# Kernel optimization log

Measured on AMD Instinct MI355X. Metric: run time of the kernel, lower is better.

Reference implementation:

```python
import jax, jax.numpy as jnp
import numpy as np

B, T, C, H = 4, 4096, 1024, 16


def setup_inputs() -> dict:
    key = jax.random.key(0)
    k1, k2, k3 = jax.random.split(key, 3)
    x = jax.random.normal(k1, (B, T, C), dtype=jnp.float32)
    # nn.Linear(d_model, 3*d_model, bias=False): weight shape [3C, C]
    W_qkv = jax.random.normal(k2, (3 * C, C), dtype=jnp.float32) * 0.02
    # output Linear(d_model, d_model): weight [C, C], bias [C]
    W_out = jax.random.normal(k3, (C, C), dtype=jnp.float32) * 0.02
    b_out = jnp.zeros((C,), dtype=jnp.float32)
    return {"x": x, "W_qkv": W_qkv, "W_out": W_out, "b_out": b_out}


def reference(x, W_qkv, W_out, b_out):
    Bs, Ts, Cs = x.shape
    dh = Cs // H
    scale = dh ** (-0.5)
    # qkv projection: [B,T,3C]
    qkv = x @ W_qkv.T
    q, k, v = jnp.split(qkv, 3, axis=-1)

    def to_heads(t):  # [B,T,C] -> [B,H,T,dh]
        return t.reshape(Bs, Ts, H, dh).transpose(0, 2, 1, 3)

    q, k, v = to_heads(q), to_heads(k), to_heads(v)
    # rfft over the sequence dim -> [B,H,F,dh], F = T//2+1 (complex64)
    q_f = jnp.fft.rfft(q, axis=-2)
    k_f = jnp.fft.rfft(k, axis=-2)
    # spectral score: sum over head_dim of conj(q)*k, real part -> [B,H,F]
    attn = jnp.sum(jnp.conj(q_f) * k_f, axis=-1).real * scale
    attn = jax.nn.softmax(attn, axis=-1)  # softmax over frequency bins
    v_f = jnp.fft.rfft(v, axis=-2)
    out = jnp.fft.irfft(attn[..., None] * v_f, n=Ts, axis=-2)  # [B,H,T,dh]
    out = out.transpose(0, 2, 1, 3).reshape(Bs, Ts, Cs)
    # output projection (dropout is identity in eval)
    return out @ W_out.T + b_out
```

## Files before the change

### kernel.cpp

```cpp
#include <hip/hip_runtime.h>
#include <math.h>

#define Bsz   4
#define Tsz   4096
#define Csz   1024
#define Hn    16
#define DHn   64
#define NTOT  (Bsz * Tsz)
#define M3    (3 * Csz)
#define Fn    2049
#define BHn   (Bsz * Hn)
#define HALFN 8192

typedef __bf16 bf16x8 __attribute__((ext_vector_type(8)));
typedef __bf16 bf16x4 __attribute__((ext_vector_type(4)));
typedef float  f32x4  __attribute__((ext_vector_type(4)));

#define VMCNT(n) asm volatile("s_waitcnt vmcnt(" #n ")" ::: "memory")

__device__ __forceinline__ void gload_lds16(const void* g, void* l) {
  __builtin_amdgcn_global_load_lds(
      (const __attribute__((address_space(1))) void*)g,
      (__attribute__((address_space(3))) void*)l, 16, 0, 0);
}

__global__ __launch_bounds__(256)
void cvt_hilo_kernel(const float4* __restrict__ in, bf16x4* __restrict__ hi,
                     bf16x4* __restrict__ lo, int n4) {
  int i = blockIdx.x * blockDim.x + threadIdx.x;
  if (i >= n4) return;
  float4 v = in[i];
  bf16x4 h, l;
  h[0] = (__bf16)v.x; h[1] = (__bf16)v.y; h[2] = (__bf16)v.z; h[3] = (__bf16)v.w;
  l[0] = (__bf16)(v.x - (float)h[0]);
  l[1] = (__bf16)(v.y - (float)h[1]);
  l[2] = (__bf16)(v.z - (float)h[2]);
  l[3] = (__bf16)(v.w - (float)h[3]);
  hi[i] = h;
  lo[i] = l;
}

__global__ __launch_bounds__(256)
void transpose_cvt_kernel(const float* __restrict__ src,
                          __bf16* __restrict__ hi, __bf16* __restrict__ lo) {
  __shared__ float tile[64][65];
  const int tid = threadIdx.x;
  const int n0 = blockIdx.x * 64;
  const int c0 = blockIdx.y * 64;
  const int col = tid & 63;
  const int row4 = tid >> 6;
#pragma unroll
  for (int i = 0; i < 16; ++i) {
    const int r = i * 4 + row4;
    tile[r][col] = src[(size_t)(c0 + r) * NTOT + n0 + col];
  }
  __syncthreads();
#pragma unroll
  for (int i = 0; i < 16; ++i) {
    const int n = i * 4 + row4;
    const float v = tile[col][n];
    const __bf16 h = (__bf16)v;
    const __bf16 l = (__bf16)(v - (float)h);
    hi[(size_t)(n0 + n) * Csz + c0 + col] = h;
    lo[(size_t)(n0 + n) * Csz + c0 + col] = l;
  }
}

template<int COLMAP>
__global__ __launch_bounds__(512, 2)
void gemm_8s(const __bf16* __restrict__ Ahi, const __bf16* __restrict__ Alo,
             const __bf16* __restrict__ Bhi, const __bf16* __restrict__ Blo,
             float* __restrict__ C, int ldC, int nbase,
             const float* __restrict__ bias) {
  __shared__ __align__(16) char lds[131072];

  const int tid  = threadIdx.x;
  const int wid  = tid >> 6;
  const int lane = tid & 63;
  const int wm = wid >> 2, wn = wid & 3;

  int bx = blockIdx.x, by = blockIdx.y;
  {
    const int gx = gridDim.x, gy = gridDim.y;
    const int nwg = gx * gy;
    if ((nwg & 7) == 0) {
      const int flat  = by * gx + bx;
      const int chunk = nwg >> 3;
      const int nf    = (flat & 7) * chunk + (flat >> 3);
      if (COLMAP) { bx = nf / gy; by = nf % gy; }
      else        { bx = nf % gx; by = nf / gx; }
    }
  }
  const int m0 = by * 256;
  const int n0 = bx * 256;

  const int r16 = lane & 15;
  const int kc  = lane >> 4;

  const int aq = (wid & 3) + ((wid & 4) ? 4 : 0);
  const int bq = ((wid & 3) << 1) + (wid >> 2);
  const __bf16* gAh = Ahi + (size_t)(m0 + (wid & 3) * 16 + ((wid & 4) ? 128 : 0) + r16) * Csz + kc * 8;
  const __bf16* gAl = Alo + (size_t)(m0 + (wid & 3) * 16 + ((wid & 4) ? 128 : 0) + r16) * Csz + kc * 8;
  const __bf16* gBh = Bhi + (size_t)(n0 + (wid & 3) * 64 + (wid >> 2) * 16 + r16) * Csz + kc * 8;
  const __bf16* gBl = Blo + (size_t)(n0 + (wid & 3) * 64 + (wid >> 2) * 16 + r16) * Csz + kc * 8;

  auto stA = [&](int h, int ts, char* slot) {
    const size_t o = (size_t)h * 64 * Csz + ts * 32;
    gload_lds16(gAh + o, slot + aq * 1024);
    gload_lds16(gAl + o, slot + 8192 + aq * 1024);
  };
  auto stB = [&](int h, int ts, char* slot) {
    const size_t o = (size_t)h * 32 * Csz + ts * 32;
    gload_lds16(gBh + o, slot + bq * 1024);
    gload_lds16(gBl + o, slot + 8192 + bq * 1024);
  };

  f32x4 acc[8][4];
#pragma unroll
  for (int i = 0; i < 8; ++i)
#pragma unroll
    for (int j = 0; j < 4; ++j) acc[i][j] = (f32x4)(0.f);

  stA(0, 0, lds);            stB(0, 0, lds + 16384);
  stB(1, 0, lds + 32768);    stA(1, 0, lds + 49152);
  stA(0, 1, lds + 65536);    stB(0, 1, lds + 81920);

#pragma unroll 1
  for (int t = 0; t < 32; ++t) {
    char* cur = lds + ((t & 1) << 16);
    char* nxt = lds + (((t & 1) ^ 1) << 16);
    bf16x8 ah[4], al[4], bh[4], bl[4];

    if (t < 31) { VMCNT(8); } else { VMCNT(4); }
    __builtin_amdgcn_s_barrier();
#pragma unroll
    for (int f = 0; f < 4; ++f) {
      const int off = (wm * 4 + f) * 1024 + lane * 16;
      ah[f] = *(const bf16x8*)(cur + off);
      al[f] = *(const bf16x8*)(cur + 8192 + off);
    }
#pragma unroll
    for (int j = 0; j < 2; ++j) {
      const int off = ((wn << 1) + j) * 1024 + lane * 16;
      bh[j] = *(const bf16x8*)(cur + 16384 + off);
      bl[j] = *(const bf16x8*)(cur + 16384 + 8192 + off);
    }
    if (t < 31) stB(1, t + 1, nxt + 32768);
    __builtin_amdgcn_s_setprio(1);
#pragma unroll
    for (int f = 0; f < 4; ++f)
#pragma unroll
      for (int j = 0; j < 2; ++j) {
        f32x4 a_ = acc[f][j];
        a_ = __builtin_amdgcn_mfma_f32_16x16x32_bf16(ah[f], bh[j], a_, 0, 0, 0);
        a_ = __builtin_amdgcn_mfma_f32_16x16x32_bf16(ah[f], bl[j], a_, 0, 0, 0);
        a_ = __builtin_amdgcn_mfma_f32_16x16x32_bf16(al[f], bh[j], a_, 0, 0, 0);
        acc[f][j] = a_;
      }
    __builtin_amdgcn_s_setprio(0);

    if (t < 31) { VMCNT(8); } else { VMCNT(2); }
    __builtin_amdgcn_s_barrier();
#pragma unroll
    for (int j = 0; j < 2; ++j) {
      const int off = ((wn << 1) + j) * 1024 + lane * 16;
      bh[2 + j] = *(const bf16x8*)(cur + 32768 + off);
      bl[2 + j] = *(const bf16x8*)(cur + 32768 + 8192 + off);
    }
    if (t < 31) stA(1, t + 1, nxt + 49152);
    __builtin_amdgcn_s_setprio(1);
#pragma unroll
    for (int f = 0; f < 4; ++f)
#pragma unroll
      for (int j = 0; j < 2; ++j) {
        f32x4 a_ = acc[f][2 + j];
        a_ = __builtin_amdgcn_mfma_f32_16x16x32_bf16(ah[f], bh[2 + j], a_, 0, 0, 0);
        a_ = __builtin_amdgcn_mfma_f32_16x16x32_bf16(ah[f], bl[2 + j], a_, 0, 0, 0);
        a_ = __builtin_amdgcn_mfma_f32_16x16x32_bf16(al[f], bh[2 + j], a_, 0, 0, 0);
        acc[f][2 + j] = a_;
      }
    __builtin_amdgcn_s_setprio(0);

    if (t < 31) { VMCNT(8); } else { VMCNT(0); }
    __builtin_amdgcn_s_barrier();
#pragma unroll
    for (int f = 0; f < 4; ++f) {
      const int off = (wm * 4 + f) * 1024 + lane * 16;
      ah[f] = *(const bf16x8*)(cur + 49152 + off);
      al[f] = *(const bf16x8*)(cur + 49152 + 8192 + off);
    }
    if (t < 30) stA(0, t + 2, cur);
    __builtin_amdgcn_s_setprio(1);
#pragma unroll
    for (int f = 0; f < 4; ++f)
#pragma unroll
      for (int j = 0; j < 2; ++j) {
        f32x4 a_ = acc[4 + f][j];
        a_ = __builtin_amdgcn_mfma_f32_16x16x32_bf16(ah[f], bh[j], a_, 0, 0, 0);
        a_ = __builtin_amdgcn_mfma_f32_16x16x32_bf16(ah[f], bl[j], a_, 0, 0, 0);
        a_ = __builtin_amdgcn_mfma_f32_16x16x32_bf16(al[f], bh[j], a_, 0, 0, 0);
        acc[4 + f][j] = a_;
      }
    __builtin_amdgcn_s_setprio(0);
    if (t < 30) stB(0, t + 2, cur + 16384);
    __builtin_amdgcn_s_setprio(1);
#pragma unroll
    for (int f = 0; f < 4; ++f)
#pragma unroll
      for (int j = 0; j < 2; ++j) {
        f32x4 a_ = acc[4 + f][2 + j];
        a_ = __builtin_amdgcn_mfma_f32_16x16x32_bf16(ah[f], bh[2 + j], a_, 0, 0, 0);
        a_ = __builtin_amdgcn_mfma_f32_16x16x32_bf16(ah[f], bl[2 + j], a_, 0, 0, 0);
        a_ = __builtin_amdgcn_mfma_f32_16x16x32_bf16(al[f], bh[2 + j], a_, 0, 0, 0);
        acc[4 + f][2 + j] = a_;
      }
    __builtin_amdgcn_s_setprio(0);
  }

  const int cm = m0 + wm * 128 + (lane >> 4) * 4;
  const int cn = nbase + n0 + wn * 64 + (lane & 15);
  float bb[4];
#pragma unroll
  for (int g = 0; g < 4; ++g) bb[g] = bias ? bias[cn - nbase + g * 16] : 0.f;
#pragma unroll
  for (int fm = 0; fm < 8; ++fm)
#pragma unroll
    for (int r = 0; r < 4; ++r) {
      float* cp = C + (size_t)(cm + fm * 16 + r) * ldC + cn;
#pragma unroll
      for (int g = 0; g < 4; ++g) cp[g * 16] = acc[fm][g][r] + bb[g];
    }
}

template<int COLMAP>
__global__ __launch_bounds__(512, 2)
void gemm_8s4(const __bf16* __restrict__ Ahi, const __bf16* __restrict__ Alo,
              const __bf16* __restrict__ Bhi, const __bf16* __restrict__ Blo,
              float* __restrict__ C, int ldC, int nbase,
              const float* __restrict__ bias) {
  __shared__ __align__(16) char lds[98304];

  const int tid  = threadIdx.x;
  const int wid  = tid >> 6;
  const int lane = tid & 63;
  const int wm = wid >> 2, wn = wid & 3;

  int bx = blockIdx.x, by = blockIdx.y;
  {
    const int gx = gridDim.x, gy = gridDim.y;
    const int nwg = gx * gy;
    if ((nwg & 7) == 0) {
      const int flat  = by * gx + bx;
      const int chunk = nwg >> 3;
      const int nf    = (flat & 7) * chunk + (flat >> 3);
      if (COLMAP) { bx = nf / gy; by = nf % gy; }
      else        { bx = nf % gx; by = nf / gx; }
    }
  }
  const int m0 = by * 128;
  const int n0 = bx * 256;

  const int r16 = lane & 15;
  const int kc  = lane >> 4;

  const int cw = wid & 3;
  const __bf16* gA = ((wid & 4) ? Alo : Ahi) +
      (size_t)(m0 + (cw >> 1) * 64 + (cw & 1) * 16 + r16) * Csz + kc * 8;
  const int adst = ((wid & 4) ? 4096 : 0) + cw * 1024;
  const int bq = ((wid & 3) << 1) + (wid >> 2);
  const __bf16* gBh = Bhi + (size_t)(n0 + (wid & 3) * 64 + (wid >> 2) * 16 + r16) * Csz + kc * 8;
  const __bf16* gBl = Blo + (size_t)(n0 + (wid & 3) * 64 + (wid >> 2) * 16 + r16) * Csz + kc * 8;

  auto stA = [&](int h, int ts, char* slot) {
    gload_lds16(gA + (size_t)h * 32 * Csz + ts * 32, slot + adst);
  };
  auto stB = [&](int h, int ts, char* slot) {
    const size_t o = (size_t)h * 32 * Csz + ts * 32;
    gload_lds16(gBh + o, slot + bq * 1024);
    gload_lds16(gBl + o, slot + 8192 + bq * 1024);
  };

  f32x4 acc[4][4];
#pragma unroll
  for (int i = 0; i < 4; ++i)
#pragma unroll
    for (int j = 0; j < 4; ++j) acc[i][j] = (f32x4)(0.f);

  stA(0, 0, lds);            stB(0, 0, lds + 8192);
  stB(1, 0, lds + 24576);    stA(1, 0, lds + 40960);
  stA(0, 1, lds + 49152);    stB(0, 1, lds + 49152 + 8192);

#pragma unroll 1
  for (int t = 0; t < 32; ++t) {
    char* cur = lds + (t & 1) * 49152;
    char* nxt = lds + ((t & 1) ^ 1) * 49152;
    bf16x8 ah[2], al[2], bh[4], bl[4];

    if (t < 31) { VMCNT(6); } else { VMCNT(3); }
    __builtin_amdgcn_s_barrier();
#pragma unroll
    for (int f = 0; f < 2; ++f) {
      const int off = (wm * 2 + f) * 1024 + lane * 16;
      ah[f] = *(const bf16x8*)(cur + off);
      al[f] = *(const bf16x8*)(cur + 4096 + off);
    }
#pragma unroll
    for (int j = 0; j < 2; ++j) {
      const int off = ((wn << 1) + j) * 1024 + lane * 16;
      bh[j] = *(const bf16x8*)(cur + 8192 + off);
      bl[j] = *(const bf16x8*)(cur + 8192 + 8192 + off);
    }
    if (t < 31) stB(1, t + 1, nxt + 24576);
    __builtin_amdgcn_s_setprio(1);
#pragma unroll
    for (int f = 0; f < 2; ++f)
#pragma unroll
      for (int j = 0; j < 2; ++j) {
        f32x4 a_ = acc[f][j];
        a_ = __builtin_amdgcn_mfma_f32_16x16x32_bf16(ah[f], bh[j], a_, 0, 0, 0);
        a_ = __builtin_amdgcn_mfma_f32_16x16x32_bf16(ah[f], bl[j], a_, 0, 0, 0);
        a_ = __builtin_amdgcn_mfma_f32_16x16x32_bf16(al[f], bh[j], a_, 0, 0, 0);
        acc[f][j] = a_;
      }
    __builtin_amdgcn_s_setprio(0);

    if (t < 31) { VMCNT(6); } else { VMCNT(1); }
    __builtin_amdgcn_s_barrier();
#pragma unroll
    for (int j = 0; j < 2; ++j) {
      const int off = ((wn << 1) + j) * 1024 + lane * 16;
      bh[2 + j] = *(const bf16x8*)(cur + 24576 + off);
      bl[2 + j] = *(const bf16x8*)(cur + 24576 + 8192 + off);
    }
    if (t < 31) stA(1, t + 1, nxt + 40960);
    __builtin_amdgcn_s_setprio(1);
#pragma unroll
    for (int f = 0; f < 2; ++f)
#pragma unroll
      for (int j = 0; j < 2; ++j) {
        f32x4 a_ = acc[f][2 + j];
        a_ = __builtin_amdgcn_mfma_f32_16x16x32_bf16(ah[f], bh[2 + j], a_, 0, 0, 0);
        a_ = __builtin_amdgcn_mfma_f32_16x16x32_bf16(ah[f], bl[2 + j], a_, 0, 0, 0);
        a_ = __builtin_amdgcn_mfma_f32_16x16x32_bf16(al[f], bh[2 + j], a_, 0, 0, 0);
        acc[f][2 + j] = a_;
      }
    __builtin_amdgcn_s_setprio(0);

    if (t < 31) { VMCNT(6); } else { VMCNT(0); }
    __builtin_amdgcn_s_barrier();
#pragma unroll
    for (int f = 0; f < 2; ++f) {
      const int off = (wm * 2 + f) * 1024 + lane * 16;
      ah[f] = *(const bf16x8*)(cur + 40960 + off);
      al[f] = *(const bf16x8*)(cur + 40960 + 4096 + off);
    }
    if (t < 30) stA(0, t + 2, cur);
    __builtin_amdgcn_s_setprio(1);
#pragma unroll
    for (int f = 0; f < 2; ++f)
#pragma unroll
      for (int j = 0; j < 2; ++j) {
        f32x4 a_ = acc[2 + f][j];
        a_ = __builtin_amdgcn_mfma_f32_16x16x32_bf16(ah[f], bh[j], a_, 0, 0, 0);
        a_ = __builtin_amdgcn_mfma_f32_16x16x32_bf16(ah[f], bl[j], a_, 0, 0, 0);
        a_ = __builtin_amdgcn_mfma_f32_16x16x32_bf16(al[f], bh[j], a_, 0, 0, 0);
        acc[2 + f][j] = a_;
      }
    __builtin_amdgcn_s_setprio(0);
    if (t < 30) stB(0, t + 2, cur + 8192);
    __builtin_amdgcn_s_setprio(1);
#pragma unroll
    for (int f = 0; f < 2; ++f)
#pragma unroll
      for (int j = 0; j < 2; ++j) {
        f32x4 a_ = acc[2 + f][2 + j];
        a_ = __builtin_amdgcn_mfma_f32_16x16x32_bf16(ah[f], bh[2 + j], a_, 0, 0, 0);
        a_ = __builtin_amdgcn_mfma_f32_16x16x32_bf16(ah[f], bl[2 + j], a_, 0, 0, 0);
        a_ = __builtin_amdgcn_mfma_f32_16x16x32_bf16(al[f], bh[2 + j], a_, 0, 0, 0);
        acc[2 + f][2 + j] = a_;
      }
    __builtin_amdgcn_s_setprio(0);
  }

  const int cm = m0 + wm * 64 + (lane >> 4) * 4;
  const int cn = nbase + n0 + wn * 64 + (lane & 15);
  float bb[4];
#pragma unroll
  for (int g = 0; g < 4; ++g) bb[g] = bias ? bias[cn - nbase + g * 16] : 0.f;
#pragma unroll
  for (int fm = 0; fm < 4; ++fm)
#pragma unroll
    for (int r = 0; r < 4; ++r) {
      float* cp = C + (size_t)(cm + fm * 16 + r) * ldC + cn;
#pragma unroll
      for (int g = 0; g < 4; ++g) cp[g * 16] = acc[fm][g][r] + bb[g];
    }
}

__device__ __forceinline__ void build_twiddle512(float2* tw, int tid) {
  const float k = 6.28318530717958647692f / 4096.0f;
#pragma unroll
  for (int i = 0; i < 2; ++i) {
    const int e = tid + i * 512;
    float sn, cs;
    __sincosf(k * (float)e, &sn, &cs);
    tw[e] = make_float2(cs, sn);
  }
}

__device__ __forceinline__ float2 cmul(float2 a, float2 b) {
  return make_float2(a.x * b.x - a.y * b.y, a.x * b.y + a.y * b.x);
}

__device__ __forceinline__ void fft4096_r4p(float2* X, float2* Y,
                                            const float2* __restrict__ tw,
                                            int tid, float sign) {
  float2* src = X;
  float2* dst = Y;
#pragma unroll 1
  for (int stage = 0; stage < 6; ++stage) {
    const int s = 1 << (2 * stage);
    __syncthreads();
    const int i0 = tid << 1;
    float4 A0 = *(const float4*)(src + i0);
    float4 A1 = *(const float4*)(src + i0 + 1024);
    float4 A2 = *(const float4*)(src + i0 + 2048);
    float4 A3 = *(const float4*)(src + i0 + 3072);
    float2 y[2][4];
#pragma unroll
    for (int e = 0; e < 2; ++e) {
      const float2 a0 = e ? make_float2(A0.z, A0.w) : make_float2(A0.x, A0.y);
      const float2 a1 = e ? make_float2(A1.z, A1.w) : make_float2(A1.x, A1.y);
      const float2 a2 = e ? make_float2(A2.z, A2.w) : make_float2(A2.x, A2.y);
      const float2 a3 = e ? make_float2(A3.z, A3.w) : make_float2(A3.x, A3.y);
      float2 b0 = make_float2(a0.x + a2.x, a0.y + a2.y);
      float2 b1 = make_float2(a0.x - a2.x, a0.y - a2.y);
      float2 b2 = make_float2(a1.x + a3.x, a1.y + a3.y);
      float2 b3 = make_float2(a1.x - a3.x, a1.y - a3.y);
      y[e][0] = make_float2(b0.x + b2.x, b0.y + b2.y);
      y[e][2] = make_float2(b0.x - b2.x, b0.y - b2.y);
      y[e][1] = make_float2(b1.x - sign * b3.y, b1.y + sign * b3.x);
      y[e][3] = make_float2(b1.x + sign * b3.y, b1.y - sign * b3.x);
    }
    if (stage == 0) {
#pragma unroll
      for (int e = 0; e < 2; ++e) {
        const int idx = i0 + e;
        float2 w1 = tw[idx];
        w1.y *= sign;
        float2 w2 = make_float2(w1.x * w1.x - w1.y * w1.y, 2.f * w1.x * w1.y);
        float2 w3 = cmul(w1, w2);
        float2 t1 = cmul(w1, y[e][1]);
        float2 t2 = cmul(w2, y[e][2]);
        float2 t3 = cmul(w3, y[e][3]);
        const int o = idx << 2;
        *(float4*)(dst + o)     = make_float4(y[e][0].x, y[e][0].y, t1.x, t1.y);
        *(float4*)(dst + o + 2) = make_float4(t2.x, t2.y, t3.x, t3.y);
      }
    } else {
      const int sp = i0 & ~(s - 1);
      float2 w1 = tw[sp];
      w1.y *= sign;
      float2 w2 = make_float2(w1.x * w1.x - w1.y * w1.y, 2.f * w1.x * w1.y);
      float2 w3 = cmul(w1, w2);
      const int o = i0 + 3 * sp;
      *(float4*)(dst + o) = make_float4(y[0][0].x, y[0][0].y, y[1][0].x, y[1][0].y);
      float2 p0 = cmul(w1, y[0][1]);
      float2 p1 = cmul(w1, y[1][1]);
      *(float4*)(dst + o + s) = make_float4(p0.x, p0.y, p1.x, p1.y);
      p0 = cmul(w2, y[0][2]);
      p1 = cmul(w2, y[1][2]);
      *(float4*)(dst + o + 2 * s) = make_float4(p0.x, p0.y, p1.x, p1.y);
      p0 = cmul(w3, y[0][3]);
      p1 = cmul(w3, y[1][3]);
      *(float4*)(dst + o + 3 * s) = make_float4(p0.x, p0.y, p1.x, p1.y);
    }
    float2* t = src; src = dst; dst = t;
  }
  __syncthreads();
}

__global__ __launch_bounds__(512)
void qk_cross_kernel(const float* __restrict__ qkT, float* __restrict__ attn_raw,
                     int bhbase) {
  __shared__ float2 bufA[4096];
  __shared__ float2 bufB[4096];
  __shared__ float2 twid[1024];
  const int tid = threadIdx.x;
  const int blk = blockIdx.x;
  const int d = blk & 63;
  const int bh = bhbase + (blk >> 6);
  const int h = bh & 15;
  const int b = bh >> 4;

  build_twiddle512(twid, tid);

  const float4* qrow = (const float4*)(qkT + (size_t)(h * DHn + d) * NTOT + b * Tsz);
  const float4* krow = (const float4*)(qkT + (size_t)(Csz + h * DHn + d) * NTOT + b * Tsz);
#pragma unroll
  for (int i = 0; i < 2; ++i) {
    const int t4 = tid + (i << 9);
    float4 qv = qrow[t4];
    float4 kv = krow[t4];
    bufA[t4 * 4 + 0] = make_float2(qv.x, kv.x);
    bufA[t4 * 4 + 1] = make_float2(qv.y, kv.y);
    bufA[t4 * 4 + 2] = make_float2(qv.z, kv.z);
    bufA[t4 * 4 + 3] = make_float2(qv.w, kv.w);
  }

  fft4096_r4p(bufA, bufB, twid, tid, -1.0f);

  float* outp = attn_raw + (size_t)bh * Fn;
  for (int f = tid; f < Fn; f += 512) {
    float2 zf = bufA[f];
    float2 zn = bufA[(4096 - f) & 4095];
    float ar = zf.x + zn.x;
    float ai = zf.y - zn.y;
    float br = zf.x - zn.x;
    float bi = zf.y + zn.y;
    float val = 0.03125f * (ar * bi - ai * br);
    atomicAdd(&outp[f], val);
  }
}

__global__ __launch_bounds__(256)
void softmax_kernel(const float* __restrict__ raw, float* __restrict__ attn) {
  __shared__ float red[256];
  const int tid = threadIdx.x;
  const float* in = raw + (size_t)blockIdx.x * Fn;
  float* outp = attn + (size_t)blockIdx.x * Fn;

  float lmax = -3.4e38f;
  for (int f = tid; f < Fn; f += 256) lmax = fmaxf(lmax, in[f]);
  red[tid] = lmax;
  __syncthreads();
  for (int off = 128; off > 0; off >>= 1) {
    if (tid < off) red[tid] = fmaxf(red[tid], red[tid + off]);
    __syncthreads();
  }
  const float mx = red[0];
  __syncthreads();

  float lsum = 0.f;
  for (int f = tid; f < Fn; f += 256) lsum += __expf(in[f] - mx);
  red[tid] = lsum;
  __syncthreads();
  for (int off = 128; off > 0; off >>= 1) {
    if (tid < off) red[tid] += red[tid + off];
    __syncthreads();
  }
  const float inv = 1.0f / red[0];
  for (int f = tid; f < Fn; f += 256) outp[f] = __expf(in[f] - mx) * inv;
}

__global__ __launch_bounds__(512)
void v_filter_kernel(const float* __restrict__ vT, float* __restrict__ vbarT,
                     const float* __restrict__ attn) {
  __shared__ float2 bufA[4096];
  __shared__ float2 bufB[4096];
  __shared__ float2 twid[1024];
  const int tid = threadIdx.x;
  const int blk = blockIdx.x;
  const int jp = blk & 31;
  const int bh = blk >> 5;
  const int h = bh & 15;
  const int b = bh >> 4;
  const int d0 = jp * 2;

  build_twiddle512(twid, tid);

  const float4* v0 = (const float4*)(vT + (size_t)(h * DHn + d0) * NTOT + b * Tsz);
  const float4* v1 = (const float4*)(vT + (size_t)(h * DHn + d0 + 1) * NTOT + b * Tsz);
#pragma unroll
  for (int i = 0; i < 2; ++i) {
    const int t4 = tid + (i << 9);
    float4 av = v0[t4];
    float4 bv = v1[t4];
    bufA[t4 * 4 + 0] = make_float2(av.x, bv.x);
    bufA[t4 * 4 + 1] = make_float2(av.y, bv.y);
    bufA[t4 * 4 + 2] = make_float2(av.z, bv.z);
    bufA[t4 * 4 + 3] = make_float2(av.w, bv.w);
  }

  fft4096_r4p(bufA, bufB, twid, tid, -1.0f);

  const float* a = attn + (size_t)bh * Fn;
  for (int f = tid; f < 4096; f += 512) {
    int fm = (f <= 2048) ? f : (4096 - f);
    float s = a[fm];
    float2 z = bufA[f];
    bufA[f] = make_float2(z.x * s, z.y * s);
  }

  fft4096_r4p(bufA, bufB, twid, tid, +1.0f);

  float* y0 = vbarT + (size_t)(h * DHn + d0) * NTOT + b * Tsz;
  float* y1 = y0 + NTOT;
  const float inv = 1.0f / 4096.0f;
  for (int t = tid; t < 4096; t += 512) {
    float2 z = bufA[t];
    y0[t] = z.x * inv;
    y1[t] = z.y * inv;
  }
}

__global__ void zero_kernel(float* __restrict__ p, int n) {
  int i = blockIdx.x * blockDim.x + threadIdx.x;
  if (i < n) p[i] = 0.f;
}

extern "C" void kernel_launch(void* const* d_in, const int* in_sizes, int n_in,
                              void* d_out, int out_size, void* d_ws, size_t ws_size,
                              hipStream_t stream) {
  const float* x    = (const float*)d_in[0];
  const float* Wqkv = (const float*)d_in[1];
  const float* Wout = (const float*)d_in[2];
  const float* bout = (const float*)d_in[3];
  float* out = (float*)d_out;

  char* ws = (char*)d_ws;
  float* qkT      = (float*)ws;
  float* vT       = (float*)ws;
  __bf16* VThi    = (__bf16*)ws;
  __bf16* VTlo    = (__bf16*)(ws + 33554432ull);
  float* vbarT    = (float*)(ws + 67108864ull);
  float* attn_raw = (float*)(ws + 134217728ull);
  float* attn     = (float*)(ws + 134742272ull);
  __bf16* Whi     = (__bf16*)(ws + 135266816ull);
  __bf16* Wlo     = (__bf16*)(ws + 141558272ull);
  __bf16* Xhi     = (__bf16*)(ws + 147849728ull);
  __bf16* Xlo     = (__bf16*)(ws + 164626944ull);
  __bf16* Wouthi  = (__bf16*)(ws + 181404160ull);
  __bf16* Woutlo  = (__bf16*)(ws + 183501312ull);

  const int nraw = BHn * Fn;
  zero_kernel<<<(nraw + 255) / 256, 256, 0, stream>>>(attn_raw, nraw);

  cvt_hilo_kernel<<<3072, 256, 0, stream>>>((const float4*)Wqkv,
                                            (bf16x4*)Whi, (bf16x4*)Wlo, 786432);
  cvt_hilo_kernel<<<1024, 256, 0, stream>>>((const float4*)Wout,
                                            (bf16x4*)Wouthi, (bf16x4*)Woutlo, 262144);

  for (int half = 0; half < 2; ++half) {
    cvt_hilo_kernel<<<8192, 256, 0, stream>>>(
        (const float4*)(x + (size_t)half * HALFN * Csz),
        (bf16x4*)Xhi, (bf16x4*)Xlo, 2097152);
    gemm_8s<1><<<dim3(32, 8), 512, 0, stream>>>(Whi, Wlo, Xhi, Xlo,
                                                qkT, NTOT, half * HALFN, nullptr);
    qk_cross_kernel<<<2048, 512, 0, stream>>>(qkT, attn_raw, half * 32);
    gemm_8s4<1><<<dim3(32, 8), 512, 0, stream>>>(Whi + 2048 * Csz, Wlo + 2048 * Csz,
                                                 Xhi, Xlo, vT, NTOT, half * HALFN,
                                                 nullptr);
  }

  softmax_kernel<<<BHn, 256, 0, stream>>>(attn_raw, attn);

  v_filter_kernel<<<2048, 512, 0, stream>>>(vT, vbarT, attn);

  transpose_cvt_kernel<<<dim3(NTOT / 64, Csz / 64), 256, 0, stream>>>(vbarT, VThi, VTlo);

  gemm_8s<0><<<dim3(4, 64), 512, 0, stream>>>(VThi, VTlo, Wouthi, Woutlo,
                                              out, Csz, 0, bout);
}
```

Measured before the change: 552.7 us.

## Replace double-buffered LDS pipeline with single-buffer quadrant reuse in split-bf16 GEMMs

Both GEMM kernels drop the two-stage LDS ping-pong and keep one set of four quadrant slots. Each slot is refilled for the next k-step as soon as its current contents are read into registers, with new vmcnt thresholds. This halves LDS use (128KB to 64KB and 96KB to 48KB), and launch bounds are raised to ask for more resident blocks per CU. The cost is a shallower prefetch distance, so global-load latency is hidden less and the barriers are more likely to stall. Register pressure from the 8x4 accumulators may also block the higher occupancy.

```diff
diff --git a/kernel.cpp b/kernel.cpp
--- a/kernel.cpp
+++ b/kernel.cpp
@@ -67,12 +67,12 @@
 }
 
 template<int COLMAP>
-__global__ __launch_bounds__(512, 2)
+__global__ __launch_bounds__(512, 4)
 void gemm_8s(const __bf16* __restrict__ Ahi, const __bf16* __restrict__ Alo,
              const __bf16* __restrict__ Bhi, const __bf16* __restrict__ Blo,
              float* __restrict__ C, int ldC, int nbase,
              const float* __restrict__ bias) {
-  __shared__ __align__(16) char lds[131072];
+  __shared__ __align__(16) char lds[65536];
 
   const int tid  = threadIdx.x;
   const int wid  = tid >> 6;
@@ -121,31 +121,29 @@
 #pragma unroll
     for (int j = 0; j < 4; ++j) acc[i][j] = (f32x4)(0.f);
 
-  stA(0, 0, lds);            stB(0, 0, lds + 16384);
-  stB(1, 0, lds + 32768);    stA(1, 0, lds + 49152);
-  stA(0, 1, lds + 65536);    stB(0, 1, lds + 81920);
+  stA(0, 0, lds);
+  stB(0, 0, lds + 16384);
+  stB(1, 0, lds + 32768);
 
 #pragma unroll 1
   for (int t = 0; t < 32; ++t) {
-    char* cur = lds + ((t & 1) << 16);
-    char* nxt = lds + (((t & 1) ^ 1) << 16);
     bf16x8 ah[4], al[4], bh[4], bl[4];
 
-    if (t < 31) { VMCNT(8); } else { VMCNT(4); }
+    VMCNT(2);
     __builtin_amdgcn_s_barrier();
 #pragma unroll
     for (int f = 0; f < 4; ++f) {
       const int off = (wm * 4 + f) * 1024 + lane * 16;
-      ah[f] = *(const bf16x8*)(cur + off);
-      al[f] = *(const bf16x8*)(cur + 8192 + off);
+      ah[f] = *(const bf16x8*)(lds + off);
+      al[f] = *(const bf16x8*)(lds + 8192 + off);
     }
 #pragma unroll
     for (int j = 0; j < 2; ++j) {
       const int off = ((wn << 1) + j) * 1024 + lane * 16;
-      bh[j] = *(const bf16x8*)(cur + 16384 + off);
-      bl[j] = *(const bf16x8*)(cur + 16384 + 8192 + off);
-    }
-    if (t < 31) stB(1, t + 1, nxt + 32768);
+      bh[j] = *(const bf16x8*)(lds + 16384 + off);
+      bl[j] = *(const bf16x8*)(lds + 16384 + 8192 + off);
+    }
+    stA(1, t, lds + 49152);
     __builtin_amdgcn_s_setprio(1);
 #pragma unroll
     for (int f = 0; f < 4; ++f)
@@ -159,15 +157,15 @@
       }
     __builtin_amdgcn_s_setprio(0);
 
-    if (t < 31) { VMCNT(8); } else { VMCNT(2); }
+    VMCNT(2);
     __builtin_amdgcn_s_barrier();
 #pragma unroll
     for (int j = 0; j < 2; ++j) {
       const int off = ((wn << 1) + j) * 1024 + lane * 16;
-      bh[2 + j] = *(const bf16x8*)(cur + 32768 + off);
-      bl[2 + j] = *(const bf16x8*)(cur + 32768 + 8192 + off);
-    }
-    if (t < 31) stA(1, t + 1, nxt + 49152);
+      bh[2 + j] = *(const bf16x8*)(lds + 32768 + off);
+      bl[2 + j] = *(const bf16x8*)(lds + 32768 + 8192 + off);
+    }
+    if (t < 31) { stA(0, t + 1, lds); stB(0, t + 1, lds + 16384); }
     __builtin_amdgcn_s_setprio(1);
 #pragma unroll
     for (int f = 0; f < 4; ++f)
@@ -181,15 +179,15 @@
       }
     __builtin_amdgcn_s_setprio(0);
 
-    if (t < 31) { VMCNT(8); } else { VMCNT(0); }
+    if (t < 31) { VMCNT(4); } else { VMCNT(0); }
     __builtin_amdgcn_s_barrier();
 #pragma unroll
     for (int f = 0; f < 4; ++f) {
       const int off = (wm * 4 + f) * 1024 + lane * 16;
-      ah[f] = *(const bf16x8*)(cur + 49152 + off);
-      al[f] = *(const bf16x8*)(cur + 49152 + 8192 + off);
-    }
-    if (t < 30) stA(0, t + 2, cur);
+      ah[f] = *(const bf16x8*)(lds + 49152 + off);
+      al[f] = *(const bf16x8*)(lds + 49152 + 8192 + off);
+    }
+    if (t < 31) stB(1, t + 1, lds + 32768);
     __builtin_amdgcn_s_setprio(1);
 #pragma unroll
     for (int f = 0; f < 4; ++f)
@@ -201,9 +199,6 @@
         a_ = __builtin_amdgcn_mfma_f32_16x16x32_bf16(al[f], bh[j], a_, 0, 0, 0);
         acc[4 + f][j] = a_;
       }
-    __builtin_amdgcn_s_setprio(0);
-    if (t < 30) stB(0, t + 2, cur + 16384);
-    __builtin_amdgcn_s_setprio(1);
 #pragma unroll
     for (int f = 0; f < 4; ++f)
 #pragma unroll
@@ -233,12 +228,12 @@
 }
 
 template<int COLMAP>
-__global__ __launch_bounds__(512, 2)
+__global__ __launch_bounds__(512, 4)
 void gemm_8s4(const __bf16* __restrict__ Ahi, const __bf16* __restrict__ Alo,
               const __bf16* __restrict__ Bhi, const __bf16* __restrict__ Blo,
               float* __restrict__ C, int ldC, int nbase,
               const float* __restrict__ bias) {
-  __shared__ __align__(16) char lds[98304];
+  __shared__ __align__(16) char lds[49152];
 
   const int tid  = threadIdx.x;
   const int wid  = tid >> 6;
@@ -286,31 +281,29 @@
 #pragma unroll
     for (int j = 0; j < 4; ++j) acc[i][j] = (f32x4)(0.f);
 
-  stA(0, 0, lds);            stB(0, 0, lds + 8192);
-  stB(1, 0, lds + 24576);    stA(1, 0, lds + 40960);
-  stA(0, 1, lds + 49152);    stB(0, 1, lds + 49152 + 8192);
+  stA(0, 0, lds);
+  stB(0, 0, lds + 8192);
+  stB(1, 0, lds + 24576);
 
 #pragma unroll 1
   for (int t = 0; t < 32; ++t) {
-    char* cur = lds + (t & 1) * 49152;
-    char* nxt = lds + ((t & 1) ^ 1) * 49152;
     bf16x8 ah[2], al[2], bh[4], bl[4];
 
-    if (t < 31) { VMCNT(6); } else { VMCNT(3); }
+    VMCNT(2);
     __builtin_amdgcn_s_barrier();
 #pragma unroll
     for (int f = 0; f < 2; ++f) {
       const int off = (wm * 2 + f) * 1024 + lane * 16;
-      ah[f] = *(const bf16x8*)(cur + off);
-      al[f] = *(const bf16x8*)(cur + 4096 + off);
+      ah[f] = *(const bf16x8*)(lds + off);
+      al[f] = *(const bf16x8*)(lds + 4096 + off);
     }
 #pragma unroll
     for (int j = 0; j < 2; ++j) {
       const int off = ((wn << 1) + j) * 1024 + lane * 16;
-      bh[j] = *(const bf16x8*)(cur + 8192 + off);
-      bl[j] = *(const bf16x8*)(cur + 8192 + 8192 + off);
-    }
-    if (t < 31) stB(1, t + 1, nxt + 24576);
+      bh[j] = *(const bf16x8*)(lds + 8192 + off);
+      bl[j] = *(const bf16x8*)(lds + 8192 + 8192 + off);
+    }
+    stA(1, t, lds + 40960);
     __builtin_amdgcn_s_setprio(1);
 #pragma unroll
     for (int f = 0; f < 2; ++f)
@@ -324,15 +317,15 @@
       }
     __builtin_amdgcn_s_setprio(0);
 
-    if (t < 31) { VMCNT(6); } else { VMCNT(1); }
+    VMCNT(1);
     __builtin_amdgcn_s_barrier();
 #pragma unroll
     for (int j = 0; j < 2; ++j) {
       const int off = ((wn << 1) + j) * 1024 + lane * 16;
-      bh[2 + j] = *(const bf16x8*)(cur + 24576 + off);
-      bl[2 + j] = *(const bf16x8*)(cur + 24576 + 8192 + off);
-    }
-    if (t < 31) stA(1, t + 1, nxt + 40960);
+      bh[2 + j] = *(const bf16x8*)(lds + 24576 + off);
+      bl[2 + j] = *(const bf16x8*)(lds + 24576 + 8192 + off);
+    }
+    if (t < 31) { stA(0, t + 1, lds); stB(0, t + 1, lds + 8192); }
     __builtin_amdgcn_s_setprio(1);
 #pragma unroll
     for (int f = 0; f < 2; ++f)
@@ -346,15 +339,15 @@
       }
     __builtin_amdgcn_s_setprio(0);
 
-    if (t < 31) { VMCNT(6); } else { VMCNT(0); }
+    if (t < 31) { VMCNT(3); } else { VMCNT(0); }
     __builtin_amdgcn_s_barrier();
 #pragma unroll
     for (int f = 0; f < 2; ++f) {
       const int off = (wm * 2 + f) * 1024 + lane * 16;
-      ah[f] = *(const bf16x8*)(cur + 40960 + off);
-      al[f] = *(const bf16x8*)(cur + 40960 + 4096 + off);
-    }
-    if (t < 30) stA(0, t + 2, cur);
+      ah[f] = *(const bf16x8*)(lds + 40960 + off);
+      al[f] = *(const bf16x8*)(lds + 40960 + 4096 + off);
+    }
+    if (t < 31) stB(1, t + 1, lds + 24576);
     __builtin_amdgcn_s_setprio(1);
 #pragma unroll
     for (int f = 0; f < 2; ++f)
@@ -366,9 +359,6 @@
         a_ = __builtin_amdgcn_mfma_f32_16x16x32_bf16(al[f], bh[j], a_, 0, 0, 0);
         acc[2 + f][j] = a_;
       }
-    __builtin_amdgcn_s_setprio(0);
-    if (t < 30) stB(0, t + 2, cur + 8192);
-    __builtin_amdgcn_s_setprio(1);
 #pragma unroll
     for (int f = 0; f < 2; ++f)
 #pragma unroll
```

Result: slower. 1.700 ms (+207.6%).
